# Optimization experiments

Hardware: AMD Instinct MI355X
Metric: run time of the kernel (lower is better)

Reference implementation:

```python
import jax, jax.numpy as jnp
import numpy as np

N = 100000
E = 600000
H = 128
OUT = 64
L = 3

def glorot(key, shape):
    fan_in, fan_out = shape[0], shape[1]
    lim = jnp.sqrt(6.0 / (fan_in + fan_out))
    return jax.random.uniform(key, shape, jnp.float32, -lim, lim)

def setup_inputs() -> dict:
    key = jax.random.key(0)
    ks = jax.random.split(key, 20)
    x = jax.random.normal(ks[0], (N, H), jnp.float32)
    edge_index = jax.random.randint(ks[1], (2, E), 0, N, jnp.int64)
    edge_attr = jax.random.uniform(ks[2], (E, 1), jnp.float32)
    # stacked per-layer params [L, ...]
    W_lin = jnp.stack([glorot(jax.random.fold_in(ks[3], i), (H, H)) for i in range(L)])
    b_lin = jnp.zeros((L, H), jnp.float32)
    W_msg = jnp.stack([glorot(jax.random.fold_in(ks[4], i), (H + 1, H)) for i in range(L)])
    b_msg = jnp.zeros((L, H), jnp.float32)
    W_l = jnp.stack([glorot(jax.random.fold_in(ks[5], i), (H, H)) for i in range(L)])
    b_l = jnp.zeros((L, H), jnp.float32)
    W_r = jnp.stack([glorot(jax.random.fold_in(ks[6], i), (H, H)) for i in range(L)])
    W_dec = glorot(ks[7], (H, H))
    b_dec = jnp.zeros((H,), jnp.float32)
    W_fin = glorot(ks[8], (H, OUT))
    b_fin = jnp.zeros((OUT,), jnp.float32)
    return {"x": x, "edge_attr": edge_attr, "W_lin": W_lin, "b_lin": b_lin,
            "W_msg": W_msg, "b_msg": b_msg, "W_l": W_l, "b_l": b_l, "W_r": W_r,
            "W_dec": W_dec, "b_dec": b_dec, "W_fin": W_fin, "b_fin": b_fin,
            "edge_index": edge_index}

def reference(x, edge_attr, W_lin, b_lin, W_msg, b_msg, W_l, b_l, W_r,
              W_dec, b_dec, W_fin, b_fin, edge_index):
    src, dst = edge_index[0], edge_index[1]  # j -> i (source_to_target)
    # mean-aggregation denominator: in-degree clamped to 1
    deg = jax.ops.segment_sum(jnp.ones((E,), jnp.float32), dst, num_segments=N)
    inv_deg = (1.0 / jnp.maximum(deg, 1.0))[:, None]  # [N,1]
    for l in range(L):
        h = jax.nn.relu(x @ W_lin[l] + b_lin[l])          # [N,H]
        msg_in = jnp.concatenate([h[src], edge_attr], -1)  # [E,H+1]
        msg = jax.nn.relu(msg_in @ W_msg[l] + b_msg[l])    # [E,H]
        agg = jax.ops.segment_sum(msg, dst, num_segments=N) * inv_deg  # [N,H]
        out = (agg @ W_l[l] + b_l[l]) + x @ W_r[l]         # lin_l(agg) + lin_r(x_r)
        x = jax.nn.relu(out)  # dropout p=0.0 -> identity
    emb = jax.nn.relu(x @ W_dec + b_dec)
    logits = emb @ W_fin + b_fin  # [N,OUT]
    return logits
```

## Files before the change

### kernel.cpp

```cpp
#include <hip/hip_runtime.h>

using short8 = __attribute__((ext_vector_type(8))) short;
using f32x4  = __attribute__((ext_vector_type(4))) float;

constexpr int HD = 128;

__device__ __forceinline__ unsigned short f2bf(float f) {
    unsigned u = __builtin_bit_cast(unsigned, f);
    u += 0x7fffu + ((u >> 16) & 1u);
    return (unsigned short)(u >> 16);
}
__device__ __forceinline__ float bflo(unsigned u) { return __builtin_bit_cast(float, u << 16); }
__device__ __forceinline__ float bfhi(unsigned u) { return __builtin_bit_cast(float, u & 0xffff0000u); }

__device__ __forceinline__ short8 ldg8(const unsigned short* p) {
    return *reinterpret_cast<const short8*>(p);
}

template<bool DUAL, bool CHAIN, int NC2, bool F32OUT>
__global__ __launch_bounds__(256)
void k_gemm_s(const unsigned short* __restrict__ A1, const unsigned short* __restrict__ Wt1,
              const unsigned short* __restrict__ A2, const unsigned short* __restrict__ Wt2,
              const unsigned short* __restrict__ Wtc, const float* __restrict__ b1,
              const float* __restrict__ b2, void* __restrict__ Out, int nrows)
{
    __shared__ __align__(16) unsigned short As1[64 * HD];
    __shared__ __align__(16) unsigned short As2[DUAL ? 64 * HD : 8];
    __shared__ __align__(16) unsigned short Hs [CHAIN ? 64 * HD : 8];

    const int tid  = threadIdx.x;
    const int lane = tid & 63, wave = tid >> 6;
    const int lr = lane & 15, lg = lane >> 4;
    const int row0 = blockIdx.x * 64;

#pragma unroll
    for (int it = 0; it < 4; ++it) {
        const int q   = wave * 4 + it;
        const int c   = q * 64 + lane;
        const int row = c >> 4, cw = c & 15;
        int grow = row0 + row; grow = grow < nrows ? grow : nrows - 1;
        const int gco = (cw ^ (row & 7)) << 3;
        __builtin_amdgcn_global_load_lds((const unsigned int*)(A1 + (long)grow * HD + gco),
                                         (unsigned int*)&As1[q * 512], 16, 0, 0);
        if constexpr (DUAL)
            __builtin_amdgcn_global_load_lds((const unsigned int*)(A2 + (long)grow * HD + gco),
                                             (unsigned int*)&As2[q * 512], 16, 0, 0);
    }

    const int cb1 = wave * 32;
    short8 bf1[2][4];
#pragma unroll
    for (int ct = 0; ct < 2; ++ct) {
        const unsigned short* bp = Wt1 + (long)(cb1 + ct * 16 + lr) * HD + lg * 8;
#pragma unroll
        for (int kt = 0; kt < 4; ++kt) bf1[ct][kt] = ldg8(bp + kt * 32);
    }
    short8 bf2[DUAL ? 2 : 1][4];
    if constexpr (DUAL) {
#pragma unroll
        for (int ct = 0; ct < 2; ++ct) {
            const unsigned short* bp = Wt2 + (long)(cb1 + ct * 16 + lr) * HD + lg * 8;
#pragma unroll
            for (int kt = 0; kt < 4; ++kt) bf2[ct][kt] = ldg8(bp + kt * 32);
        }
    }
    constexpr int CT2 = CHAIN ? (NC2 / 64) : 1;
    const int cb2 = wave * (NC2 / 4);
    short8 bfc[CT2][4];
    if constexpr (CHAIN) {
#pragma unroll
        for (int ct = 0; ct < CT2; ++ct) {
            const unsigned short* bp = Wtc + (long)(cb2 + ct * 16 + lr) * HD + lg * 8;
#pragma unroll
            for (int kt = 0; kt < 4; ++kt) bfc[ct][kt] = ldg8(bp + kt * 32);
        }
    }

    __syncthreads();

    f32x4 acc[4][2] = {};
#pragma unroll
    for (int kt = 0; kt < 4; ++kt) {
        short8 af[4];
#pragma unroll
        for (int rt = 0; rt < 4; ++rt)
            af[rt] = *reinterpret_cast<const short8*>(
                &As1[(rt * 16 + lr) * HD + (((kt * 4 + lg) ^ (lr & 7)) << 3)]);
#pragma unroll
        for (int rt = 0; rt < 4; ++rt)
#pragma unroll
            for (int ct = 0; ct < 2; ++ct)
                acc[rt][ct] = __builtin_amdgcn_mfma_f32_16x16x32_bf16(af[rt], bf1[ct][kt], acc[rt][ct], 0, 0, 0);
        if constexpr (DUAL) {
            short8 af2[4];
#pragma unroll
            for (int rt = 0; rt < 4; ++rt)
                af2[rt] = *reinterpret_cast<const short8*>(
                    &As2[(rt * 16 + lr) * HD + (((kt * 4 + lg) ^ (lr & 7)) << 3)]);
#pragma unroll
            for (int rt = 0; rt < 4; ++rt)
#pragma unroll
                for (int ct = 0; ct < 2; ++ct)
                    acc[rt][ct] = __builtin_amdgcn_mfma_f32_16x16x32_bf16(af2[rt], bf2[ct][kt], acc[rt][ct], 0, 0, 0);
        }
    }

    const float bv1[2] = { b1[cb1 + lr], b1[cb1 + 16 + lr] };

    if constexpr (!CHAIN) {
        unsigned short* C = (unsigned short*)Out;
#pragma unroll
        for (int rt = 0; rt < 4; ++rt)
#pragma unroll
            for (int ct = 0; ct < 2; ++ct) {
                const int cc = cb1 + ct * 16 + lr;
#pragma unroll
                for (int i = 0; i < 4; ++i) {
                    const int r = row0 + rt * 16 + lg * 4 + i;
                    if (r < nrows) C[(long)r * HD + cc] = f2bf(fmaxf(acc[rt][ct][i] + bv1[ct], 0.f));
                }
            }
    } else {
#pragma unroll
        for (int rt = 0; rt < 4; ++rt)
#pragma unroll
            for (int ct = 0; ct < 2; ++ct) {
                const int cc = cb1 + ct * 16 + lr;
#pragma unroll
                for (int i = 0; i < 4; ++i) {
                    const int row = rt * 16 + lg * 4 + i;
                    const float v = fmaxf(acc[rt][ct][i] + bv1[ct], 0.f);
                    Hs[row * HD + ((((cc >> 3) ^ (row & 7)) << 3) | (cc & 7))] = f2bf(v);
                }
            }
        __syncthreads();

        f32x4 acc2[4][CT2] = {};
#pragma unroll
        for (int kt = 0; kt < 4; ++kt) {
            short8 ah[4];
#pragma unroll
            for (int rt = 0; rt < 4; ++rt)
                ah[rt] = *reinterpret_cast<const short8*>(
                    &Hs[(rt * 16 + lr) * HD + (((kt * 4 + lg) ^ (lr & 7)) << 3)]);
#pragma unroll
            for (int rt = 0; rt < 4; ++rt)
#pragma unroll
                for (int ct = 0; ct < CT2; ++ct)
                    acc2[rt][ct] = __builtin_amdgcn_mfma_f32_16x16x32_bf16(ah[rt], bfc[ct][kt], acc2[rt][ct], 0, 0, 0);
        }
        float bv2[CT2];
#pragma unroll
        for (int ct = 0; ct < CT2; ++ct) bv2[ct] = b2[cb2 + ct * 16 + lr];
#pragma unroll
        for (int rt = 0; rt < 4; ++rt)
#pragma unroll
            for (int ct = 0; ct < CT2; ++ct) {
                const int cc = cb2 + ct * 16 + lr;
#pragma unroll
                for (int i = 0; i < 4; ++i) {
                    const int r = row0 + rt * 16 + lg * 4 + i;
                    if (r < nrows) {
                        const float v = acc2[rt][ct][i] + bv2[ct];
                        if constexpr (F32OUT) ((float*)Out)[(long)r * NC2 + cc] = v;
                        else ((unsigned short*)Out)[(long)r * NC2 + cc] = f2bf(v);
                    }
                }
            }
    }
}

__global__ void k_cast_bf16(const float* __restrict__ in, unsigned short* __restrict__ out, long n8) {
    long i = (long)blockIdx.x * 256 + threadIdx.x;
    if (i >= n8) return;
    const float4 v0 = *((const float4*)in + i * 2);
    const float4 v1 = *((const float4*)in + i * 2 + 1);
    unsigned o[4];
    o[0] = (unsigned)f2bf(v0.x) | ((unsigned)f2bf(v0.y) << 16);
    o[1] = (unsigned)f2bf(v0.z) | ((unsigned)f2bf(v0.w) << 16);
    o[2] = (unsigned)f2bf(v1.x) | ((unsigned)f2bf(v1.y) << 16);
    o[3] = (unsigned)f2bf(v1.z) | ((unsigned)f2bf(v1.w) << 16);
    *(uint4*)(out + i * 8) = *(uint4*)o;
}

__global__ void k_prep_w(const float* __restrict__ Wlin, const float* __restrict__ Wmsg,
                         const float* __restrict__ Wl,   const float* __restrict__ Wr,
                         const float* __restrict__ Wdec, const float* __restrict__ Wfin,
                         unsigned short* __restrict__ wt)
{
    const int m = blockIdx.y;
    const float* src; int C = 128;
    if      (m < 3)  src = Wlin + m * 16384;
    else if (m < 6)  src = Wmsg + (m - 3) * (129 * 128);
    else if (m < 9)  src = Wl   + (m - 6) * 16384;
    else if (m < 12) src = Wr   + (m - 9) * 16384;
    else if (m == 12) src = Wdec;
    else { src = Wfin; C = 64; }
    const int elems = C * 128;
    int e = blockIdx.x * 256 + threadIdx.x;
    if (e >= elems) return;
    int c = e >> 7, k = e & 127;
    wt[m * 16384 + e] = f2bf(src[k * C + c]);
}

__global__ void k_deg(const int* __restrict__ dst, int* __restrict__ deg, int nE, int n) {
    const int grp = blockIdx.x & 7;
    const int bin = blockIdx.x >> 3;
    const int nbin = gridDim.x >> 3;
    const int chunk = (n + 7) >> 3;
    const int lo = grp * chunk;
    const int hi = min(n, lo + chunk);
    for (int e = bin * 256 + threadIdx.x; e < nE; e += nbin * 256) {
        const int d = dst[e];
        if (d >= lo && d < hi) atomicAdd(&deg[d], 1);
    }
}

__global__ void k_chunksum(const int* __restrict__ deg, int* __restrict__ csum, int n) {
    __shared__ int s[256];
    int t = threadIdx.x, i = blockIdx.x * 256 + t;
    s[t] = (i < n) ? deg[i] : 0;
    __syncthreads();
    for (int o = 128; o > 0; o >>= 1) { if (t < o) s[t] += s[t + o]; __syncthreads(); }
    if (t == 0) csum[blockIdx.x] = s[0];
}

__global__ void k_scanmid(const int* __restrict__ csum, int* __restrict__ cbase,
                          int* __restrict__ rowstart, int nch, int n) {
    __shared__ int s[512];
    int t = threadIdx.x;
    int v = (t < nch) ? csum[t] : 0;
    s[t] = v; __syncthreads();
    for (int off = 1; off < 512; off <<= 1) {
        int tmp = (t >= off) ? s[t - off] : 0;
        __syncthreads();
        s[t] += tmp;
        __syncthreads();
    }
    if (t < nch) cbase[t] = s[t] - v;
    if (t == nch - 1) rowstart[n] = s[t];
}

__global__ void k_scan2(const int* __restrict__ deg, const int* __restrict__ cbase,
                        int* __restrict__ rowstart, float* __restrict__ inv_deg, int n) {
    __shared__ int s[256];
    int t = threadIdx.x, i = blockIdx.x * 256 + t;
    int v = (i < n) ? deg[i] : 0;
    s[t] = v; __syncthreads();
    for (int off = 1; off < 256; off <<= 1) {
        int tmp = (t >= off) ? s[t - off] : 0;
        __syncthreads();
        s[t] += tmp;
        __syncthreads();
    }
    if (i < n) {
        rowstart[i] = cbase[blockIdx.x] + s[t] - v;
        inv_deg[i] = 1.0f / fmaxf((float)v, 1.0f);
    }
}

__global__ void k_fill(const int* __restrict__ src, const int* __restrict__ dst,
                       const float* __restrict__ eattr, const int* __restrict__ rowstart,
                       int* __restrict__ degcur, uint2* __restrict__ csr_rec, int nE, int n) {
    const int grp = blockIdx.x & 7;
    const int bin = blockIdx.x >> 3;
    const int nbin = gridDim.x >> 3;
    const int chunk = (n + 7) >> 3;
    const int lo = grp * chunk;
    const int hi = min(n, lo + chunk);
    for (int e = bin * 256 + threadIdx.x; e < nE; e += nbin * 256) {
        const int d = dst[e];
        if (d >= lo && d < hi) {
            const int p = rowstart[d] + atomicSub(&degcur[d], 1) - 1;
            uint2 rec;
            rec.x = (unsigned)src[e];
            rec.y = __builtin_bit_cast(unsigned, eattr[e]);
            csr_rec[p] = rec;
        }
    }
}

__global__ __launch_bounds__(256)
void k_agg(const unsigned short* __restrict__ g, const uint2* __restrict__ rec,
           const int* __restrict__ rs, const float* __restrict__ inv_deg,
           const float* __restrict__ wlast, unsigned short* __restrict__ agg, int n) {
    const int lane = threadIdx.x & 15;
    const int node = blockIdx.x * 16 + (threadIdx.x >> 4);
    if (node >= n) return;
    const int c0 = lane * 8;
    const float4 wla = *(const float4*)(wlast + c0);
    const float4 wlb = *(const float4*)(wlast + c0 + 4);
    const int p0 = rs[node], p1 = rs[node + 1];
    float a0=0,a1=0,a2=0,a3=0,a4=0,a5=0,a6=0,a7=0;
    int p = p0;
    for (; p + 4 <= p1; p += 4) {
        uint2 r[4];
#pragma unroll
        for (int u = 0; u < 4; ++u) r[u] = rec[p + u];
        uint4 G[4];
#pragma unroll
        for (int u = 0; u < 4; ++u) G[u] = *(const uint4*)(g + (long)r[u].x * HD + c0);
#pragma unroll
        for (int u = 0; u < 4; ++u) {
            const float e = __builtin_bit_cast(float, r[u].y);
            a0 += fmaxf(fmaf(e, wla.x, bflo(G[u].x)), 0.f);
            a1 += fmaxf(fmaf(e, wla.y, bfhi(G[u].x)), 0.f);
            a2 += fmaxf(fmaf(e, wla.z, bflo(G[u].y)), 0.f);
            a3 += fmaxf(fmaf(e, wla.w, bfhi(G[u].y)), 0.f);
            a4 += fmaxf(fmaf(e, wlb.x, bflo(G[u].z)), 0.f);
            a5 += fmaxf(fmaf(e, wlb.y, bfhi(G[u].z)), 0.f);
            a6 += fmaxf(fmaf(e, wlb.z, bflo(G[u].w)), 0.f);
            a7 += fmaxf(fmaf(e, wlb.w, bfhi(G[u].w)), 0.f);
        }
    }
    for (; p < p1; ++p) {
        const uint2 r0 = rec[p];
        const float e0 = __builtin_bit_cast(float, r0.y);
        const uint4 G0 = *(const uint4*)(g + (long)r0.x * HD + c0);
        a0 += fmaxf(fmaf(e0, wla.x, bflo(G0.x)), 0.f);
        a1 += fmaxf(fmaf(e0, wla.y, bfhi(G0.x)), 0.f);
        a2 += fmaxf(fmaf(e0, wla.z, bflo(G0.y)), 0.f);
        a3 += fmaxf(fmaf(e0, wla.w, bfhi(G0.y)), 0.f);
        a4 += fmaxf(fmaf(e0, wlb.x, bflo(G0.z)), 0.f);
        a5 += fmaxf(fmaf(e0, wlb.y, bfhi(G0.z)), 0.f);
        a6 += fmaxf(fmaf(e0, wlb.z, bflo(G0.w)), 0.f);
        a7 += fmaxf(fmaf(e0, wlb.w, bfhi(G0.w)), 0.f);
    }
    const float id = inv_deg[node];
    uint4 o;
    o.x = (unsigned)f2bf(a0 * id) | ((unsigned)f2bf(a1 * id) << 16);
    o.y = (unsigned)f2bf(a2 * id) | ((unsigned)f2bf(a3 * id) << 16);
    o.z = (unsigned)f2bf(a4 * id) | ((unsigned)f2bf(a5 * id) << 16);
    o.w = (unsigned)f2bf(a6 * id) | ((unsigned)f2bf(a7 * id) << 16);
    *(uint4*)(agg + (long)node * HD + c0) = o;
}

extern "C" void kernel_launch(void* const* d_in, const int* in_sizes, int n_in,
                              void* d_out, int out_size, void* d_ws, size_t ws_size,
                              hipStream_t stream)
{
    const float* x     = (const float*)d_in[0];
    const float* eattr = (const float*)d_in[1];
    const float* W_lin = (const float*)d_in[2];
    const float* b_lin = (const float*)d_in[3];
    const float* W_msg = (const float*)d_in[4];
    const float* b_msg = (const float*)d_in[5];
    const float* W_l   = (const float*)d_in[6];
    const float* b_l   = (const float*)d_in[7];
    const float* W_r   = (const float*)d_in[8];
    const float* W_dec = (const float*)d_in[9];
    const float* b_dec = (const float*)d_in[10];
    const float* W_fin = (const float*)d_in[11];
    const float* b_fin = (const float*)d_in[12];
    const int*   ei    = (const int*)d_in[13];

    const int N = in_sizes[0] / HD;
    const int E = in_sizes[1];
    const int* srcv = ei;
    const int* dstv = ei + E;

    char* wsb = (char*)d_ws;
    size_t off = 0;
    auto carve = [&](size_t bytes) -> void* {
        void* p = wsb + off;
        off += (bytes + 255) & ~(size_t)255;
        return p;
    };
    unsigned short* xb = (unsigned short*)carve((size_t)N * HD * 2);
    unsigned short* t1 = (unsigned short*)carve((size_t)N * HD * 2);
    unsigned short* t2 = (unsigned short*)carve((size_t)N * HD * 2);
    unsigned short* t3 = (unsigned short*)carve((size_t)N * HD * 2);
    unsigned short* wt = (unsigned short*)carve((size_t)14 * 16384 * 2);
    uint2* csr_rec  = (uint2*)carve((size_t)E * 8);
    int*   rowstart = (int*)carve((size_t)(N + 1) * 4);
    int*   deg      = (int*)carve((size_t)N * 4);
    float* inv_deg  = (float*)carve((size_t)N * 4);
    const int NCH = (N + 255) / 256;
    int* csum  = (int*)carve((size_t)NCH * 4);
    int* cbase = (int*)carve((size_t)NCH * 4);

    if (off > ws_size) {
        hipMemsetAsync(d_out, 0, (size_t)out_size * 4, stream);
        return;
    }

    hipMemsetAsync(deg, 0, (size_t)N * 4, stream);

    k_cast_bf16<<<(int)(((long)N * HD / 8 + 255) / 256), 256, 0, stream>>>(x, xb, (long)N * HD / 8);
    k_prep_w<<<dim3(64, 14), 256, 0, stream>>>(W_lin, W_msg, W_l, W_r, W_dec, W_fin, wt);

    k_deg<<<2048, 256, 0, stream>>>(dstv, deg, E, N);
    k_chunksum<<<NCH, 256, 0, stream>>>(deg, csum, N);
    k_scanmid<<<1, 512, 0, stream>>>(csum, cbase, rowstart, NCH, N);
    k_scan2<<<NCH, 256, 0, stream>>>(deg, cbase, rowstart, inv_deg, N);
    k_fill<<<2048, 256, 0, stream>>>(srcv, dstv, eattr, rowstart, deg, csr_rec, E, N);

    auto WT = [&](int m) { return wt + (size_t)m * 16384; };
    const int NB64 = (N + 63) / 64;
    const int GAGG = (N + 15) / 16;

    const unsigned short* xin = xb;
    for (int l = 0; l < 3; ++l) {
        unsigned short* gb = (l == 1) ? t3 : t2;
        k_gemm_s<false, true, 128, false><<<NB64, 256, 0, stream>>>(
            xin, WT(l), nullptr, nullptr, WT(3 + l), b_lin + l * HD, b_msg + l * HD, gb, N);
        k_agg<<<GAGG, 256, 0, stream>>>(
            gb, csr_rec, rowstart, inv_deg,
            W_msg + (size_t)l * (HD + 1) * HD + (size_t)HD * HD, t1, N);
        k_gemm_s<true, false, 128, false><<<NB64, 256, 0, stream>>>(
            t1, WT(6 + l), xin, WT(9 + l), nullptr, b_l + l * HD, nullptr, gb, N);
        xin = gb;
    }
    k_gemm_s<false, true, 64, true><<<NB64, 256, 0, stream>>>(
        xin, WT(12), nullptr, nullptr, WT(13), b_dec, b_fin, (float*)d_out, N);
}
```

Before: 355.0 us.

## Merge independent prep kernels into shared launches and fuse final layer with decoder

Degree counting, the x→bf16 cast and weight transposition now run as block ranges of one launch. The CSR fill runs in one launch alongside the first layer's chained GEMM, so independent work can overlap and fewer kernels are launched. The last layer's dual GEMM is fused with the decoder and final projection, so the final node embeddings never round-trip through global memory. In exchange the fused decoder kernel uses three 16 KB LDS tiles, which may lower occupancy, and the mixed-role grids can imbalance scheduling.

```diff
diff --git a/kernel.cpp b/kernel.cpp
--- a/kernel.cpp
+++ b/kernel.cpp
@@ -4,6 +4,7 @@
 using f32x4  = __attribute__((ext_vector_type(4))) float;
 
 constexpr int HD = 128;
+constexpr int NBLK_SCAT = 2048;
 
 __device__ __forceinline__ unsigned short f2bf(float f) {
     unsigned u = __builtin_bit_cast(unsigned, f);
@@ -17,16 +18,130 @@
     return *reinterpret_cast<const short8*>(p);
 }
 
-template<bool DUAL, bool CHAIN, int NC2, bool F32OUT>
+template<int NC2, bool F32OUT>
+__device__ __forceinline__ void dev_chain(unsigned short* As1, unsigned short* Hs,
+    const unsigned short* __restrict__ A, const unsigned short* __restrict__ Wt1,
+    const unsigned short* __restrict__ Wtc, const float* __restrict__ b1,
+    const float* __restrict__ b2, void* __restrict__ Out, int nrows, int bid)
+{
+    const int tid  = threadIdx.x;
+    const int lane = tid & 63, wave = tid >> 6;
+    const int lr = lane & 15, lg = lane >> 4;
+    const int row0 = bid * 64;
+
+#pragma unroll
+    for (int it = 0; it < 4; ++it) {
+        const int q   = wave * 4 + it;
+        const int c   = q * 64 + lane;
+        const int row = c >> 4, cw = c & 15;
+        int grow = row0 + row; grow = grow < nrows ? grow : nrows - 1;
+        const int gco = (cw ^ (row & 7)) << 3;
+        __builtin_amdgcn_global_load_lds((const unsigned int*)(A + (long)grow * HD + gco),
+                                         (unsigned int*)&As1[q * 512], 16, 0, 0);
+    }
+
+    const int cb1 = wave * 32;
+    short8 bf1[2][4];
+#pragma unroll
+    for (int ct = 0; ct < 2; ++ct) {
+        const unsigned short* bp = Wt1 + (long)(cb1 + ct * 16 + lr) * HD + lg * 8;
+#pragma unroll
+        for (int kt = 0; kt < 4; ++kt) bf1[ct][kt] = ldg8(bp + kt * 32);
+    }
+    constexpr int CT2 = NC2 / 64;
+    const int cb2 = wave * (NC2 / 4);
+    short8 bfc[CT2][4];
+#pragma unroll
+    for (int ct = 0; ct < CT2; ++ct) {
+        const unsigned short* bp = Wtc + (long)(cb2 + ct * 16 + lr) * HD + lg * 8;
+#pragma unroll
+        for (int kt = 0; kt < 4; ++kt) bfc[ct][kt] = ldg8(bp + kt * 32);
+    }
+
+    __syncthreads();
+
+    f32x4 acc[4][2] = {};
+#pragma unroll
+    for (int kt = 0; kt < 4; ++kt) {
+        short8 af[4];
+#pragma unroll
+        for (int rt = 0; rt < 4; ++rt)
+            af[rt] = *reinterpret_cast<const short8*>(
+                &As1[(rt * 16 + lr) * HD + (((kt * 4 + lg) ^ (lr & 7)) << 3)]);
+#pragma unroll
+        for (int rt = 0; rt < 4; ++rt)
+#pragma unroll
+            for (int ct = 0; ct < 2; ++ct)
+                acc[rt][ct] = __builtin_amdgcn_mfma_f32_16x16x32_bf16(af[rt], bf1[ct][kt], acc[rt][ct], 0, 0, 0);
+    }
+
+    const float bv1[2] = { b1[cb1 + lr], b1[cb1 + 16 + lr] };
+#pragma unroll
+    for (int rt = 0; rt < 4; ++rt)
+#pragma unroll
+        for (int ct = 0; ct < 2; ++ct) {
+            const int cc = cb1 + ct * 16 + lr;
+#pragma unroll
+            for (int i = 0; i < 4; ++i) {
+                const int row = rt * 16 + lg * 4 + i;
+                const float v = fmaxf(acc[rt][ct][i] + bv1[ct], 0.f);
+                Hs[row * HD + ((((cc >> 3) ^ (row & 7)) << 3) | (cc & 7))] = f2bf(v);
+            }
+        }
+    __syncthreads();
+
+    f32x4 acc2[4][CT2] = {};
+#pragma unroll
+    for (int kt = 0; kt < 4; ++kt) {
+        short8 ah[4];
+#pragma unroll
+        for (int rt = 0; rt < 4; ++rt)
+            ah[rt] = *reinterpret_cast<const short8*>(
+                &Hs[(rt * 16 + lr) * HD + (((kt * 4 + lg) ^ (lr & 7)) << 3)]);
+#pragma unroll
+        for (int rt = 0; rt < 4; ++rt)
+#pragma unroll
+            for (int ct = 0; ct < CT2; ++ct)
+                acc2[rt][ct] = __builtin_amdgcn_mfma_f32_16x16x32_bf16(ah[rt], bfc[ct][kt], acc2[rt][ct], 0, 0, 0);
+    }
+    float bv2[CT2];
+#pragma unroll
+    for (int ct = 0; ct < CT2; ++ct) bv2[ct] = b2[cb2 + ct * 16 + lr];
+#pragma unroll
+    for (int rt = 0; rt < 4; ++rt)
+#pragma unroll
+        for (int ct = 0; ct < CT2; ++ct) {
+            const int cc = cb2 + ct * 16 + lr;
+#pragma unroll
+            for (int i = 0; i < 4; ++i) {
+                const int r = row0 + rt * 16 + lg * 4 + i;
+                if (r < nrows) {
+                    const float v = acc2[rt][ct][i] + bv2[ct];
+                    if constexpr (F32OUT) ((float*)Out)[(long)r * NC2 + cc] = v;
+                    else ((unsigned short*)Out)[(long)r * NC2 + cc] = f2bf(v);
+                }
+            }
+        }
+}
+
+template<int NC2, bool F32OUT>
 __global__ __launch_bounds__(256)
-void k_gemm_s(const unsigned short* __restrict__ A1, const unsigned short* __restrict__ Wt1,
-              const unsigned short* __restrict__ A2, const unsigned short* __restrict__ Wt2,
-              const unsigned short* __restrict__ Wtc, const float* __restrict__ b1,
-              const float* __restrict__ b2, void* __restrict__ Out, int nrows)
+void k_chain(const unsigned short* __restrict__ A, const unsigned short* __restrict__ Wt1,
+             const unsigned short* __restrict__ Wtc, const float* __restrict__ b1,
+             const float* __restrict__ b2, void* __restrict__ Out, int nrows)
 {
     __shared__ __align__(16) unsigned short As1[64 * HD];
-    __shared__ __align__(16) unsigned short As2[DUAL ? 64 * HD : 8];
-    __shared__ __align__(16) unsigned short Hs [CHAIN ? 64 * HD : 8];
+    __shared__ __align__(16) unsigned short Hs [64 * HD];
+    dev_chain<NC2, F32OUT>(As1, Hs, A, Wt1, Wtc, b1, b2, Out, nrows, blockIdx.x);
+}
+
+__global__ __launch_bounds__(256)
+void k_dual(const unsigned short* __restrict__ A1, const unsigned short* __restrict__ Wt1,
+            const unsigned short* __restrict__ A2, const unsigned short* __restrict__ Wt2,
+            const float* __restrict__ bias, unsigned short* __restrict__ Out, int nrows)
+{
+    __shared__ __align__(16) unsigned short As1[64 * HD];
+    __shared__ __align__(16) unsigned short As2[64 * HD];
 
     const int tid  = threadIdx.x;
     const int lane = tid & 63, wave = tid >> 6;
@@ -42,153 +157,253 @@
         const int gco = (cw ^ (row & 7)) << 3;
         __builtin_amdgcn_global_load_lds((const unsigned int*)(A1 + (long)grow * HD + gco),
                                          (unsigned int*)&As1[q * 512], 16, 0, 0);
-        if constexpr (DUAL)
-            __builtin_amdgcn_global_load_lds((const unsigned int*)(A2 + (long)grow * HD + gco),
-                                             (unsigned int*)&As2[q * 512], 16, 0, 0);
-    }
-
-    const int cb1 = wave * 32;
-    short8 bf1[2][4];
+        __builtin_amdgcn_global_load_lds((const unsigned int*)(A2 + (long)grow * HD + gco),
+                                         (unsigned int*)&As2[q * 512], 16, 0, 0);
+    }
+
+    const int cb = wave * 32;
+    short8 bf1[2][4], bf2[2][4];
 #pragma unroll
     for (int ct = 0; ct < 2; ++ct) {
-        const unsigned short* bp = Wt1 + (long)(cb1 + ct * 16 + lr) * HD + lg * 8;
-#pragma unroll
-        for (int kt = 0; kt < 4; ++kt) bf1[ct][kt] = ldg8(bp + kt * 32);
-    }
-    short8 bf2[DUAL ? 2 : 1][4];
-    if constexpr (DUAL) {
+        const unsigned short* p1 = Wt1 + (long)(cb + ct * 16 + lr) * HD + lg * 8;
+        const unsigned short* p2 = Wt2 + (long)(cb + ct * 16 + lr) * HD + lg * 8;
+#pragma unroll
+        for (int kt = 0; kt < 4; ++kt) { bf1[ct][kt] = ldg8(p1 + kt * 32); bf2[ct][kt] = ldg8(p2 + kt * 32); }
+    }
+
+    __syncthreads();
+
+    f32x4 acc[4][2] = {};
+#pragma unroll
+    for (int kt = 0; kt < 4; ++kt) {
+        short8 af[4], ag[4];
+#pragma unroll
+        for (int rt = 0; rt < 4; ++rt) {
+            const int base = (rt * 16 + lr) * HD + (((kt * 4 + lg) ^ (lr & 7)) << 3);
+            af[rt] = *reinterpret_cast<const short8*>(&As1[base]);
+            ag[rt] = *reinterpret_cast<const short8*>(&As2[base]);
+        }
+#pragma unroll
+        for (int rt = 0; rt < 4; ++rt)
+#pragma unroll
+            for (int ct = 0; ct < 2; ++ct) {
+                acc[rt][ct] = __builtin_amdgcn_mfma_f32_16x16x32_bf16(af[rt], bf1[ct][kt], acc[rt][ct], 0, 0, 0);
+                acc[rt][ct] = __builtin_amdgcn_mfma_f32_16x16x32_bf16(ag[rt], bf2[ct][kt], acc[rt][ct], 0, 0, 0);
+            }
+    }
+
+    const float bv[2] = { bias[cb + lr], bias[cb + 16 + lr] };
+#pragma unroll
+    for (int rt = 0; rt < 4; ++rt)
 #pragma unroll
         for (int ct = 0; ct < 2; ++ct) {
-            const unsigned short* bp = Wt2 + (long)(cb1 + ct * 16 + lr) * HD + lg * 8;
-#pragma unroll
-            for (int kt = 0; kt < 4; ++kt) bf2[ct][kt] = ldg8(bp + kt * 32);
-        }
-    }
-    constexpr int CT2 = CHAIN ? (NC2 / 64) : 1;
-    const int cb2 = wave * (NC2 / 4);
-    short8 bfc[CT2][4];
-    if constexpr (CHAIN) {
-#pragma unroll
-        for (int ct = 0; ct < CT2; ++ct) {
-            const unsigned short* bp = Wtc + (long)(cb2 + ct * 16 + lr) * HD + lg * 8;
-#pragma unroll
-            for (int kt = 0; kt < 4; ++kt) bfc[ct][kt] = ldg8(bp + kt * 32);
-        }
-    }
-
+            const int cc = cb + ct * 16 + lr;
+#pragma unroll
+            for (int i = 0; i < 4; ++i) {
+                const int r = row0 + rt * 16 + lg * 4 + i;
+                if (r < nrows) Out[(long)r * HD + cc] = f2bf(fmaxf(acc[rt][ct][i] + bv[ct], 0.f));
+            }
+        }
+}
+
+__global__ __launch_bounds__(256)
+void k_dualdec(const unsigned short* __restrict__ Agg, const unsigned short* __restrict__ X,
+               const unsigned short* __restrict__ WtL, const unsigned short* __restrict__ WtR,
+               const float* __restrict__ bl_, const unsigned short* __restrict__ Wdec,
+               const float* __restrict__ bdec, const unsigned short* __restrict__ Wfin,
+               const float* __restrict__ bfin, float* __restrict__ Out, int n)
+{
+    __shared__ __align__(16) unsigned short Ag[64 * HD];
+    __shared__ __align__(16) unsigned short Xs[64 * HD];
+    __shared__ __align__(16) unsigned short Ts[64 * HD];
+
+    const int tid  = threadIdx.x;
+    const int lane = tid & 63, wave = tid >> 6;
+    const int lr = lane & 15, lg = lane >> 4;
+    const int row0 = blockIdx.x * 64;
+
+#pragma unroll
+    for (int it = 0; it < 4; ++it) {
+        const int q   = wave * 4 + it;
+        const int c   = q * 64 + lane;
+        const int row = c >> 4, cw = c & 15;
+        int grow = row0 + row; grow = grow < n ? grow : n - 1;
+        const int gco = (cw ^ (row & 7)) << 3;
+        __builtin_amdgcn_global_load_lds((const unsigned int*)(Agg + (long)grow * HD + gco),
+                                         (unsigned int*)&Ag[q * 512], 16, 0, 0);
+        __builtin_amdgcn_global_load_lds((const unsigned int*)(X + (long)grow * HD + gco),
+                                         (unsigned int*)&Xs[q * 512], 16, 0, 0);
+    }
+
+    const int cb = wave * 32;
+    short8 bl[2][4], br[2][4];
+#pragma unroll
+    for (int ct = 0; ct < 2; ++ct) {
+        const unsigned short* pl = WtL + (long)(cb + ct * 16 + lr) * HD + lg * 8;
+        const unsigned short* pr = WtR + (long)(cb + ct * 16 + lr) * HD + lg * 8;
+#pragma unroll
+        for (int kt = 0; kt < 4; ++kt) { bl[ct][kt] = ldg8(pl + kt * 32); br[ct][kt] = ldg8(pr + kt * 32); }
+    }
     __syncthreads();
 
-    f32x4 acc[4][2] = {};
-#pragma unroll
-    for (int kt = 0; kt < 4; ++kt) {
-        short8 af[4];
-#pragma unroll
-        for (int rt = 0; rt < 4; ++rt)
-            af[rt] = *reinterpret_cast<const short8*>(
-                &As1[(rt * 16 + lr) * HD + (((kt * 4 + lg) ^ (lr & 7)) << 3)]);
-#pragma unroll
-        for (int rt = 0; rt < 4; ++rt)
-#pragma unroll
-            for (int ct = 0; ct < 2; ++ct)
-                acc[rt][ct] = __builtin_amdgcn_mfma_f32_16x16x32_bf16(af[rt], bf1[ct][kt], acc[rt][ct], 0, 0, 0);
-        if constexpr (DUAL) {
-            short8 af2[4];
+    {
+        f32x4 acc[4][2] = {};
+#pragma unroll
+        for (int kt = 0; kt < 4; ++kt) {
+            short8 aa[4], ax[4];
+#pragma unroll
+            for (int rt = 0; rt < 4; ++rt) {
+                const int base = (rt * 16 + lr) * HD + (((kt * 4 + lg) ^ (lr & 7)) << 3);
+                aa[rt] = *reinterpret_cast<const short8*>(&Ag[base]);
+                ax[rt] = *reinterpret_cast<const short8*>(&Xs[base]);
+            }
 #pragma unroll
             for (int rt = 0; rt < 4; ++rt)
-                af2[rt] = *reinterpret_cast<const short8*>(
-                    &As2[(rt * 16 + lr) * HD + (((kt * 4 + lg) ^ (lr & 7)) << 3)]);
-#pragma unroll
-            for (int rt = 0; rt < 4; ++rt)
-#pragma unroll
-                for (int ct = 0; ct < 2; ++ct)
-                    acc[rt][ct] = __builtin_amdgcn_mfma_f32_16x16x32_bf16(af2[rt], bf2[ct][kt], acc[rt][ct], 0, 0, 0);
-        }
-    }
-
-    const float bv1[2] = { b1[cb1 + lr], b1[cb1 + 16 + lr] };
-
-    if constexpr (!CHAIN) {
-        unsigned short* C = (unsigned short*)Out;
+#pragma unroll
+                for (int ct = 0; ct < 2; ++ct) {
+                    acc[rt][ct] = __builtin_amdgcn_mfma_f32_16x16x32_bf16(aa[rt], bl[ct][kt], acc[rt][ct], 0, 0, 0);
+                    acc[rt][ct] = __builtin_amdgcn_mfma_f32_16x16x32_bf16(ax[rt], br[ct][kt], acc[rt][ct], 0, 0, 0);
+                }
+        }
+        const float bv[2] = { bl_[cb + lr], bl_[cb + 16 + lr] };
 #pragma unroll
         for (int rt = 0; rt < 4; ++rt)
 #pragma unroll
             for (int ct = 0; ct < 2; ++ct) {
-                const int cc = cb1 + ct * 16 + lr;
-#pragma unroll
-                for (int i = 0; i < 4; ++i) {
-                    const int r = row0 + rt * 16 + lg * 4 + i;
-                    if (r < nrows) C[(long)r * HD + cc] = f2bf(fmaxf(acc[rt][ct][i] + bv1[ct], 0.f));
-                }
-            }
-    } else {
-#pragma unroll
-        for (int rt = 0; rt < 4; ++rt)
-#pragma unroll
-            for (int ct = 0; ct < 2; ++ct) {
-                const int cc = cb1 + ct * 16 + lr;
+                const int cc = cb + ct * 16 + lr;
 #pragma unroll
                 for (int i = 0; i < 4; ++i) {
                     const int row = rt * 16 + lg * 4 + i;
-                    const float v = fmaxf(acc[rt][ct][i] + bv1[ct], 0.f);
-                    Hs[row * HD + ((((cc >> 3) ^ (row & 7)) << 3) | (cc & 7))] = f2bf(v);
+                    const float v = fmaxf(acc[rt][ct][i] + bv[ct], 0.f);
+                    Ts[row * HD + ((((cc >> 3) ^ (row & 7)) << 3) | (cc & 7))] = f2bf(v);
                 }
             }
-        __syncthreads();
-
-        f32x4 acc2[4][CT2] = {};
+    }
+    __syncthreads();
+
+    {
+        short8 bd[2][4];
+#pragma unroll
+        for (int ct = 0; ct < 2; ++ct) {
+            const unsigned short* bp = Wdec + (long)(cb + ct * 16 + lr) * HD + lg * 8;
+#pragma unroll
+            for (int kt = 0; kt < 4; ++kt) bd[ct][kt] = ldg8(bp + kt * 32);
+        }
+        f32x4 acc[4][2] = {};
 #pragma unroll
         for (int kt = 0; kt < 4; ++kt) {
             short8 ah[4];
 #pragma unroll
             for (int rt = 0; rt < 4; ++rt)
                 ah[rt] = *reinterpret_cast<const short8*>(
-                    &Hs[(rt * 16 + lr) * HD + (((kt * 4 + lg) ^ (lr & 7)) << 3)]);
+                    &Ts[(rt * 16 + lr) * HD + (((kt * 4 + lg) ^ (lr & 7)) << 3)]);
 #pragma unroll
             for (int rt = 0; rt < 4; ++rt)
 #pragma unroll
-                for (int ct = 0; ct < CT2; ++ct)
-                    acc2[rt][ct] = __builtin_amdgcn_mfma_f32_16x16x32_bf16(ah[rt], bfc[ct][kt], acc2[rt][ct], 0, 0, 0);
-        }
-        float bv2[CT2];
-#pragma unroll
-        for (int ct = 0; ct < CT2; ++ct) bv2[ct] = b2[cb2 + ct * 16 + lr];
-#pragma unroll
-        for (int rt = 0; rt < 4; ++rt)
-#pragma unroll
-            for (int ct = 0; ct < CT2; ++ct) {
-                const int cc = cb2 + ct * 16 + lr;
+                for (int ct = 0; ct < 2; ++ct)
+                    acc[rt][ct] = __builtin_amdgcn_mfma_f32_16x16x32_bf16(ah[rt], bd[ct][kt], acc[rt][ct], 0, 0, 0);
+        }
+        const float bv[2] = { bdec[cb + lr], bdec[cb + 16 + lr] };
+#pragma unroll
+        for (int rt = 0; rt < 4; ++rt)
+#pragma unroll
+            for (int ct = 0; ct < 2; ++ct) {
+                const int cc = cb + ct * 16 + lr;
 #pragma unroll
                 for (int i = 0; i < 4; ++i) {
-                    const int r = row0 + rt * 16 + lg * 4 + i;
-                    if (r < nrows) {
-                        const float v = acc2[rt][ct][i] + bv2[ct];
-                        if constexpr (F32OUT) ((float*)Out)[(long)r * NC2 + cc] = v;
-                        else ((unsigned short*)Out)[(long)r * NC2 + cc] = f2bf(v);
-                    }
+                    const int row = rt * 16 + lg * 4 + i;
+                    const float v = fmaxf(acc[rt][ct][i] + bv[ct], 0.f);
+                    Ag[row * HD + ((((cc >> 3) ^ (row & 7)) << 3) | (cc & 7))] = f2bf(v);
                 }
             }
     }
-}
-
-__global__ void k_cast_bf16(const float* __restrict__ in, unsigned short* __restrict__ out, long n8) {
-    long i = (long)blockIdx.x * 256 + threadIdx.x;
-    if (i >= n8) return;
-    const float4 v0 = *((const float4*)in + i * 2);
-    const float4 v1 = *((const float4*)in + i * 2 + 1);
-    unsigned o[4];
-    o[0] = (unsigned)f2bf(v0.x) | ((unsigned)f2bf(v0.y) << 16);
-    o[1] = (unsigned)f2bf(v0.z) | ((unsigned)f2bf(v0.w) << 16);
-    o[2] = (unsigned)f2bf(v1.x) | ((unsigned)f2bf(v1.y) << 16);
-    o[3] = (unsigned)f2bf(v1.z) | ((unsigned)f2bf(v1.w) << 16);
-    *(uint4*)(out + i * 8) = *(uint4*)o;
-}
-
-__global__ void k_prep_w(const float* __restrict__ Wlin, const float* __restrict__ Wmsg,
-                         const float* __restrict__ Wl,   const float* __restrict__ Wr,
-                         const float* __restrict__ Wdec, const float* __restrict__ Wfin,
-                         unsigned short* __restrict__ wt)
+    __syncthreads();
+
+    {
+        const int cbf = wave * 16;
+        short8 bfn[4];
+#pragma unroll
+        for (int kt = 0; kt < 4; ++kt)
+            bfn[kt] = ldg8(Wfin + (long)(cbf + lr) * HD + lg * 8 + kt * 32);
+        f32x4 acc[4] = {};
+#pragma unroll
+        for (int kt = 0; kt < 4; ++kt) {
+            short8 ah[4];
+#pragma unroll
+            for (int rt = 0; rt < 4; ++rt)
+                ah[rt] = *reinterpret_cast<const short8*>(
+                    &Ag[(rt * 16 + lr) * HD + (((kt * 4 + lg) ^ (lr & 7)) << 3)]);
+#pragma unroll
+            for (int rt = 0; rt < 4; ++rt)
+                acc[rt] = __builtin_amdgcn_mfma_f32_16x16x32_bf16(ah[rt], bfn[kt], acc[rt], 0, 0, 0);
+        }
+        const float bv = bfin[cbf + lr];
+#pragma unroll
+        for (int rt = 0; rt < 4; ++rt)
+#pragma unroll
+            for (int i = 0; i < 4; ++i) {
+                const int r = row0 + rt * 16 + lg * 4 + i;
+                if (r < n) Out[(long)r * 64 + cbf + lr] = acc[rt][i] + bv;
+            }
+    }
+}
+
+__device__ __forceinline__ void dev_deg(const int* __restrict__ dst, int* __restrict__ deg,
+                                        int nE, int n, int bid, int nblk) {
+    const int grp = bid & 7, bin = bid >> 3, nbin = nblk >> 3;
+    const int chunk = (n + 7) >> 3;
+    const int lo = grp * chunk, hi = min(n, lo + chunk);
+    for (int e = bin * 256 + threadIdx.x; e < nE; e += nbin * 256) {
+        const int d = dst[e];
+        if (d >= lo && d < hi) atomicAdd(&deg[d], 1);
+    }
+}
+
+__device__ __forceinline__ void dev_fill(const int* __restrict__ src, const int* __restrict__ dst,
+                                         const float* __restrict__ eattr, const int* __restrict__ rowstart,
+                                         int* __restrict__ degcur, uint2* __restrict__ csr_rec,
+                                         int nE, int n, int bid, int nblk) {
+    const int grp = bid & 7, bin = bid >> 3, nbin = nblk >> 3;
+    const int chunk = (n + 7) >> 3;
+    const int lo = grp * chunk, hi = min(n, lo + chunk);
+    for (int e = bin * 256 + threadIdx.x; e < nE; e += nbin * 256) {
+        const int d = dst[e];
+        if (d >= lo && d < hi) {
+            const int p = rowstart[d] + atomicSub(&degcur[d], 1) - 1;
+            uint2 rec;
+            rec.x = (unsigned)src[e];
+            rec.y = __builtin_bit_cast(unsigned, eattr[e]);
+            csr_rec[p] = rec;
+        }
+    }
+}
+
+__global__ __launch_bounds__(256)
+void k_u1(const int* __restrict__ dst, int* __restrict__ deg, int nE,
+          const float* __restrict__ xin, unsigned short* __restrict__ xb, long n8, int ncast,
+          const float* __restrict__ Wlin, const float* __restrict__ Wmsg,
+          const float* __restrict__ Wl,   const float* __restrict__ Wr,
+          const float* __restrict__ Wdec, const float* __restrict__ Wfin,
+          unsigned short* __restrict__ wt, int n)
 {
-    const int m = blockIdx.y;
+    const int bid = blockIdx.x;
+    if (bid < NBLK_SCAT) { dev_deg(dst, deg, nE, n, bid, NBLK_SCAT); return; }
+    const int b = bid - NBLK_SCAT;
+    if (b < ncast) {
+        const long i = (long)b * 256 + threadIdx.x;
+        if (i >= n8) return;
+        const float4 v0 = *((const float4*)xin + i * 2);
+        const float4 v1 = *((const float4*)xin + i * 2 + 1);
+        unsigned o[4];
+        o[0] = (unsigned)f2bf(v0.x) | ((unsigned)f2bf(v0.y) << 16);
+        o[1] = (unsigned)f2bf(v0.z) | ((unsigned)f2bf(v0.w) << 16);
+        o[2] = (unsigned)f2bf(v1.x) | ((unsigned)f2bf(v1.y) << 16);
+        o[3] = (unsigned)f2bf(v1.z) | ((unsigned)f2bf(v1.w) << 16);
+        *(uint4*)(xb + i * 8) = *(uint4*)o;
+        return;
+    }
+    const int local = b - ncast;
+    const int m = local >> 6;
     const float* src; int C = 128;
     if      (m < 3)  src = Wlin + m * 16384;
     else if (m < 6)  src = Wmsg + (m - 3) * (129 * 128);
@@ -197,23 +412,27 @@
     else if (m == 12) src = Wdec;
     else { src = Wfin; C = 64; }
     const int elems = C * 128;
-    int e = blockIdx.x * 256 + threadIdx.x;
+    const int e = (local & 63) * 256 + threadIdx.x;
     if (e >= elems) return;
-    int c = e >> 7, k = e & 127;
+    const int c = e >> 7, k = e & 127;
     wt[m * 16384 + e] = f2bf(src[k * C + c]);
 }
 
-__global__ void k_deg(const int* __restrict__ dst, int* __restrict__ deg, int nE, int n) {
-    const int grp = blockIdx.x & 7;
-    const int bin = blockIdx.x >> 3;
-    const int nbin = gridDim.x >> 3;
-    const int chunk = (n + 7) >> 3;
-    const int lo = grp * chunk;
-    const int hi = min(n, lo + chunk);
-    for (int e = bin * 256 + threadIdx.x; e < nE; e += nbin * 256) {
-        const int d = dst[e];
-        if (d >= lo && d < hi) atomicAdd(&deg[d], 1);
-    }
+__global__ __launch_bounds__(256)
+void k_u2(const int* __restrict__ src, const int* __restrict__ dst,
+          const float* __restrict__ eattr, const int* __restrict__ rowstart,
+          int* __restrict__ degcur, uint2* __restrict__ csr_rec, int nE,
+          const unsigned short* __restrict__ A, const unsigned short* __restrict__ Wt1,
+          const unsigned short* __restrict__ Wtc, const float* __restrict__ b1,
+          const float* __restrict__ b2, unsigned short* __restrict__ Out, int n)
+{
+    __shared__ __align__(16) unsigned short As1[64 * HD];
+    __shared__ __align__(16) unsigned short Hs [64 * HD];
+    if (blockIdx.x < NBLK_SCAT) {
+        dev_fill(src, dst, eattr, rowstart, degcur, csr_rec, nE, n, blockIdx.x, NBLK_SCAT);
+        return;
+    }
+    dev_chain<128, false>(As1, Hs, A, Wt1, Wtc, b1, b2, Out, n, blockIdx.x - NBLK_SCAT);
 }
 
 __global__ void k_chunksum(const int* __restrict__ deg, int* __restrict__ csum, int n) {
@@ -256,27 +475,6 @@
     if (i < n) {
         rowstart[i] = cbase[blockIdx.x] + s[t] - v;
         inv_deg[i] = 1.0f / fmaxf((float)v, 1.0f);
-    }
-}
-
-__global__ void k_fill(const int* __restrict__ src, const int* __restrict__ dst,
-                       const float* __restrict__ eattr, const int* __restrict__ rowstart,
-                       int* __restrict__ degcur, uint2* __restrict__ csr_rec, int nE, int n) {
-    const int grp = blockIdx.x & 7;
-    const int bin = blockIdx.x >> 3;
-    const int nbin = gridDim.x >> 3;
-    const int chunk = (n + 7) >> 3;
-    const int lo = grp * chunk;
-    const int hi = min(n, lo + chunk);
-    for (int e = bin * 256 + threadIdx.x; e < nE; e += nbin * 256) {
-        const int d = dst[e];
-        if (d >= lo && d < hi) {
-            const int p = rowstart[d] + atomicSub(&degcur[d], 1) - 1;
-            uint2 rec;
-            rec.x = (unsigned)src[e];
-            rec.y = __builtin_bit_cast(unsigned, eattr[e]);
-            csr_rec[p] = rec;
-        }
     }
 }
 
@@ -386,31 +584,31 @@
 
     hipMemsetAsync(deg, 0, (size_t)N * 4, stream);
 
-    k_cast_bf16<<<(int)(((long)N * HD / 8 + 255) / 256), 256, 0, stream>>>(x, xb, (long)N * HD / 8);
-    k_prep_w<<<dim3(64, 14), 256, 0, stream>>>(W_lin, W_msg, W_l, W_r, W_dec, W_fin, wt);
-
-    k_deg<<<2048, 256, 0, stream>>>(dstv, deg, E, N);
+    auto WT = [&](int m) { return wt + (size_t)m * 16384; };
+    const int NB64 = (N + 63) / 64;
+    const int GAGG = (N + 15) / 16;
+    const long n8 = (long)N * HD / 8;
+    const int ncast = (int)((n8 + 255) / 256);
+
+    k_u1<<<NBLK_SCAT + ncast + 14 * 64, 256, 0, stream>>>(
+        dstv, deg, E, x, xb, n8, ncast, W_lin, W_msg, W_l, W_r, W_dec, W_fin, wt, N);
     k_chunksum<<<NCH, 256, 0, stream>>>(deg, csum, N);
     k_scanmid<<<1, 512, 0, stream>>>(csum, cbase, rowstart, NCH, N);
     k_scan2<<<NCH, 256, 0, stream>>>(deg, cbase, rowstart, inv_deg, N);
-    k_fill<<<2048, 256, 0, stream>>>(srcv, dstv, eattr, rowstart, deg, csr_rec, E, N);
-
-    auto WT = [&](int m) { return wt + (size_t)m * 16384; };
-    const int NB64 = (N + 63) / 64;
-    const int GAGG = (N + 15) / 16;
-
-    const unsigned short* xin = xb;
-    for (int l = 0; l < 3; ++l) {
-        unsigned short* gb = (l == 1) ? t3 : t2;
-        k_gemm_s<false, true, 128, false><<<NB64, 256, 0, stream>>>(
-            xin, WT(l), nullptr, nullptr, WT(3 + l), b_lin + l * HD, b_msg + l * HD, gb, N);
-        k_agg<<<GAGG, 256, 0, stream>>>(
-            gb, csr_rec, rowstart, inv_deg,
-            W_msg + (size_t)l * (HD + 1) * HD + (size_t)HD * HD, t1, N);
-        k_gemm_s<true, false, 128, false><<<NB64, 256, 0, stream>>>(
-            t1, WT(6 + l), xin, WT(9 + l), nullptr, b_l + l * HD, nullptr, gb, N);
-        xin = gb;
-    }
-    k_gemm_s<false, true, 64, true><<<NB64, 256, 0, stream>>>(
-        xin, WT(12), nullptr, nullptr, WT(13), b_dec, b_fin, (float*)d_out, N);
-}
+
+    k_u2<<<NBLK_SCAT + NB64, 256, 0, stream>>>(
+        srcv, dstv, eattr, rowstart, deg, csr_rec, E,
+        xb, WT(0), WT(3), b_lin, b_msg, t2, N);
+
+    auto wlast = [&](int l) { return W_msg + (size_t)l * (HD + 1) * HD + (size_t)HD * HD; };
+
+    k_agg<<<GAGG, 256, 0, stream>>>(t2, csr_rec, rowstart, inv_deg, wlast(0), t1, N);
+    k_dual<<<NB64, 256, 0, stream>>>(t1, WT(6), xb, WT(9), b_l, t2, N);
+    k_chain<128, false><<<NB64, 256, 0, stream>>>(t2, WT(1), WT(4), b_lin + HD, b_msg + HD, t3, N);
+    k_agg<<<GAGG, 256, 0, stream>>>(t3, csr_rec, rowstart, inv_deg, wlast(1), t1, N);
+    k_dual<<<NB64, 256, 0, stream>>>(t1, WT(7), t2, WT(10), b_l + HD, t3, N);
+    k_chain<128, false><<<NB64, 256, 0, stream>>>(t3, WT(2), WT(5), b_lin + 2 * HD, b_msg + 2 * HD, t2, N);
+    k_agg<<<GAGG, 256, 0, stream>>>(t2, csr_rec, rowstart, inv_deg, wlast(2), t1, N);
+    k_dualdec<<<NB64, 256, 0, stream>>>(t1, t3, WT(8), WT(11), b_l + 2 * HD,
+                                        WT(12), b_dec, WT(13), b_fin, (float*)d_out, N);
+}
```

Measured after the change: 340.2 us. 1.04x faster.
